# Kernel tuning notes

Hardware: AMD Instinct MI355X
Metric: run time of the kernel (lower is better)

Reference implementation:

```python
import jax, jax.numpy as jnp
import numpy as np

N_IN = 10    # input_dim: x has 2**N_IN features
N_OUT = 10   # output_dim: output has 2**N_OUT features
RANK = 10
BATCH = 512
STD = 0.5


def setup_inputs() -> dict:
    key = jax.random.key(0)
    ks = jax.random.split(key, 5)
    x = jax.random.normal(ks[0], (BATCH, 2 ** N_IN), dtype=jnp.float32)
    # Stacked tensor-train cores; each core is (rank, 2, 2, rank) as in the torch module.
    input_cores = STD * jax.random.normal(ks[1], (N_IN, RANK, 2, 2, RANK), dtype=jnp.float32)
    output_cores = STD * jax.random.normal(ks[2], (N_OUT, RANK, 2, 2, RANK), dtype=jnp.float32)
    # central core is (2,)*(N_IN+N_OUT) in the original; stored here as the
    # equivalent (2**N_IN, 2**N_OUT) matrix (identical math, same memory layout).
    central_core = STD * jax.random.normal(ks[3], (2 ** N_IN, 2 ** N_OUT), dtype=jnp.float32)
    bias = STD * jax.random.normal(ks[4], (1, 2 ** N_OUT), dtype=jnp.float32)
    return {"x": x, "input_cores": input_cores, "output_cores": output_cores,
            "central_core": central_core, "bias": bias}


def reference(x, input_cores, output_cores, central_core, bias):
    # Tensor-wheel contraction with a fixed, precomputed path (replaces the
    # per-call greedy tensornetwork contractor). Exact same sum as the original.
    B = x.shape[0]
    n, r = input_cores.shape[0], input_cores.shape[1]
    m = output_cores.shape[0]

    # --- absorb x into the input-core chain ---
    # State S: (B, l0, C_acc, r_cur, Q_rem) where
    #   l0    = open left bond of input core 0 (closes the ring later)
    #   C_acc = accumulated central-core legs c_1..c_i (dim 2^i, c_1 most significant)
    #   Q_rem = remaining input bits of x (x bit 1 is most significant, matching reshape)
    S = jnp.einsum('bpq,lpcs->blcsq', x.reshape(B, 2, -1), input_cores[0])
    for i in range(1, n):
        _, l, C, rc, Q = S.shape
        S = S.reshape(B, l, C, rc, 2, Q // 2)
        S = jnp.einsum('blcrpq,rpds->blcdsq', S, input_cores[i]).reshape(B, l, 2 * C, r, Q // 2)
    S = S[..., 0]  # (B, l0, 2^n, r_n)

    # --- contract the central core over all input-side legs (dominant GEMM) ---
    U = jnp.einsum('blcr,cd->blrd', S, central_core)  # (B, l0, r_n, 2^m)

    # --- sweep through the output-core chain ---
    # State V: (B, l0, P_acc, r_cur, D_rem); P_acc accumulates free output legs
    # p_1..p_j (p_1 most significant), D_rem holds remaining central output legs.
    V = U.reshape(B, r, 1, r, 2 ** m)
    for j in range(m):
        _, l, P, rc, D = V.shape
        V = V.reshape(B, l, P, rc, 2, D // 2)
        V = jnp.einsum('blxrdq,rpds->blxpsq', V, output_cores[j]).reshape(B, l, 2 * P, r, D // 2)

    # --- close the ring: trace l0 (input core 0 left bond) with rgt_m ---
    out = jnp.einsum('blpl->bp', V[..., 0])  # (B, 2^m)
    return out + bias
```

## Files before the change

kernel.cpp:

```cpp
#include <hip/hip_runtime.h>
#include <cstdint>
#include <cstddef>


typedef __attribute__((ext_vector_type(8))) short short8;
typedef __attribute__((ext_vector_type(4))) float f32x4;

static __device__ __forceinline__ unsigned short f2bf(float f) {
  union { float f; unsigned int u; } v; v.f = f;
  unsigned int r = v.u + 0x7FFFu + ((v.u >> 16) & 1u);
  return (unsigned short)(r >> 16);
}
static __device__ __forceinline__ unsigned int pack2(float a, float b) {
  return (unsigned int)f2bf(a) | ((unsigned int)f2bf(b) << 16);
}

static __device__ __forceinline__ int shuf_in(int stg, int u, int dd) {
  if (stg == 0) return ((u >> 4) << 6) | (dd << 4) | ((u & 3) << 2) | ((u >> 2) & 3);
  if (stg == 1) return ((u >> 2) << 4) | (dd << 2) | (u & 3);
  return (u << 2) | dd;
}
static __device__ __forceinline__ int shuf_out(int stg, int u, int dd) {
  if (stg == 0) return (dd << 6) | ((u & 15) << 2) | (u >> 4);
  if (stg == 1) return ((u >> 4) << 6) | (dd << 4) | ((u & 3) << 2) | ((u >> 2) & 3);
  if (stg == 2) return ((u >> 2) << 4) | (dd << 2) | (u & 3);
  return (u << 2) | dd;
}

static __device__ __forceinline__ void mfma_stage80(
    const unsigned short* stc, const unsigned short* __restrict__ Bf,
    int w, int lane, int c15, int quad, f32x4 acc[4][3]) {
  short8 bfr[3][2];
  #pragma unroll
  for (int nt = 0; nt < 3; ++nt) {
    bfr[nt][0] = *(const short8*)&Bf[(nt * 2 + 0) * 512 + lane * 8];
    bfr[nt][1] = *(const short8*)&Bf[(nt * 2 + 1) * 512 + lane * 8];
  }
  #pragma unroll
  for (int rt = 0; rt < 4; ++rt) {
    const int rowA = w * 64 + rt * 16 + c15;
    const short8 a0 = *(const short8*)((const char*)stc + rowA * 80 + quad * 16);
    const int a1off = (quad == 0) ? rowA * 80 + 64 : 0;
    const short8 a1 = *(const short8*)((const char*)stc + a1off);
    #pragma unroll
    for (int nt = 0; nt < 3; ++nt) {
      f32x4 a = {0.f, 0.f, 0.f, 0.f};
      a = __builtin_amdgcn_mfma_f32_16x16x32_bf16(a0, bfr[nt][0], a, 0, 0, 0);
      a = __builtin_amdgcn_mfma_f32_16x16x32_bf16(a1, bfr[nt][1], a, 0, 0, 0);
      acc[rt][nt] = a;
    }
  }
}

template <int STG, bool INPUT>
static __device__ __forceinline__ void stage_writes80(
    unsigned short* dst, const f32x4 acc[4][3], int w, int quad,
    const int* ddv, const int* sv) {
  #pragma unroll
  for (int rt = 0; rt < 4; ++rt) {
    const int u = w * 16 + rt * 4 + quad;
    #pragma unroll
    for (int nt = 0; nt < 3; ++nt) {
      if (sv[nt] < 10) {
        const int dd = ddv[nt];
        const int row = INPUT ? shuf_in(STG, u, dd) : shuf_out(STG, u, dd);
        uint2 v;
        v.x = pack2(acc[rt][nt][0], acc[rt][nt][1]);
        v.y = pack2(acc[rt][nt][2], acc[rt][nt][3]);
        *(uint2*)((char*)dst + row * 80 + sv[nt] * 8) = v;
      }
    }
  }
}

__global__ __launch_bounds__(256) void k0_prep(
    const float* __restrict__ ic, const float* __restrict__ oc,
    const float* __restrict__ cc, unsigned short* __restrict__ Bt,
    float* __restrict__ c2x, unsigned short* __restrict__ bf1,
    unsigned short* __restrict__ bf3, unsigned short* __restrict__ bf3l) {
  const int t = threadIdx.x;
  const int bx = blockIdx.x;
  if (bx < 1024) {
    const int dly = bx;
    const int D = (dly & 3) * 256 + ((dly >> 2) & 3) * 64 + (dly >> 4);
    const int uC = (t >> 2) * 16 + (t & 3);
    ushort4 pk;
    pk.x = f2bf(cc[(size_t)(uC + 0) * 1024 + D]);
    pk.y = f2bf(cc[(size_t)(uC + 4) * 1024 + D]);
    pk.z = f2bf(cc[(size_t)(uC + 8) * 1024 + D]);
    pk.w = f2bf(cc[(size_t)(uC + 12) * 1024 + D]);
    *(ushort4*)&Bt[(size_t)dly * 1024 + 4 * t] = pk;
  } else if (bx == 1024) {
    for (int idx = t; idx < 1600; idx += 256) {
      int L = idx / 160, rem = idx - L * 160;
      int w = rem / 40, r2 = rem - w * 40;
      int pi = r2 / 10, s = r2 - pi * 10;
      int p1 = pi >> 1, p2 = pi & 1, c1 = w >> 1, c2v = w & 1;
      float a = 0.f;
      for (int r1 = 0; r1 < 10; ++r1)
        a += ic[L * 40 + p1 * 20 + c1 * 10 + r1] *
             ic[400 + r1 * 40 + p2 * 20 + c2v * 10 + s];
      c2x[idx] = a;
    }
  } else if (bx == 1025) {
    for (int idx = t; idx < 12288; idx += 256) {
      int j = idx & 7, lane = (idx >> 3) & 63, kc = (idx >> 9) & 1;
      int g2 = idx >> 10, stg = g2 / 3, nt = g2 - stg * 3;
      int c15 = lane & 15, quad = lane >> 4;
      int n = nt * 16 + c15, dd = n / 12, s = n - dd * 12;
      int k = kc * 32 + quad * 8 + j, c = k >> 2, pi = k & 3;
      float v = 0.f;
      if (k < 40 && s < 10) {
        int p1 = pi >> 1, p2 = pi & 1, d1 = dd >> 1, d2 = dd & 1;
        const float* A = ic + (2 * stg + 2) * 400;
        const float* B = ic + (2 * stg + 3) * 400;
        for (int tt = 0; tt < 10; ++tt)
          v += A[c * 40 + p1 * 20 + d1 * 10 + tt] *
               B[tt * 40 + p2 * 20 + d2 * 10 + s];
      }
      bf1[idx] = f2bf(v);
    }
  } else if (bx == 1026) {
    for (int idx = t; idx < 12288; idx += 256) {
      int j = idx & 7, lane = (idx >> 3) & 63, kc = (idx >> 9) & 1;
      int g2 = idx >> 10, stg = g2 / 3, nt = g2 - stg * 3;
      int c15 = lane & 15, quad = lane >> 4;
      int n = nt * 16 + c15, dd = n / 12, s = n - dd * 12;
      int k = kc * 32 + quad * 8 + j, c = k >> 2, pi = k & 3;
      float v = 0.f;
      if (k < 40 && s < 10) {
        int d1 = pi >> 1, d2 = pi & 1, p1 = dd >> 1, p2 = dd & 1;
        const float* A = oc + (2 * stg) * 400;
        const float* B = oc + (2 * stg + 1) * 400;
        for (int tt = 0; tt < 10; ++tt)
          v += A[c * 40 + p1 * 20 + d1 * 10 + tt] *
               B[tt * 40 + p2 * 20 + d2 * 10 + s];
      }
      bf3[idx] = f2bf(v);
    }
  } else {
    for (int idx = t; idx < 10240; idx += 256) {
      int j = idx & 7, lane = (idx >> 3) & 63, kc = (idx >> 9) & 1, L = idx >> 10;
      int c15 = lane & 15, quad = lane >> 4;
      int k = kc * 32 + quad * 8 + j, c = k >> 2, pi = k & 3;
      float v = 0.f;
      if (k < 40 && c15 < 4) {
        int dd = c15, d1 = pi >> 1, d2 = pi & 1, p1 = dd >> 1, p2 = dd & 1;
        for (int tt = 0; tt < 10; ++tt)
          v += oc[8 * 400 + c * 40 + p1 * 20 + d1 * 10 + tt] *
               oc[9 * 400 + tt * 40 + p2 * 20 + d2 * 10 + L];
      }
      bf3l[idx] = f2bf(v);
    }
  }
}

__global__ __launch_bounds__(256, 4) void k1_insweep(
    const float* __restrict__ x, const float* __restrict__ c2x,
    const unsigned short* __restrict__ bf1, unsigned short* __restrict__ S) {
  __shared__ __align__(16) unsigned short st[20480];
  const int t = threadIdx.x, bx = blockIdx.x;
  const int b = bx / 10, L = bx - b * 10;
  const int lane = t & 63, w = t >> 6;
  const int c15 = lane & 15, quad = lane >> 4;
  int ddv[3], sv[3];
  #pragma unroll
  for (int nt = 0; nt < 3; ++nt) {
    int n = nt * 16 + c15; ddv[nt] = n / 12; sv[nt] = n - ddv[nt] * 12;
  }
  unsigned short* bufA = st;
  unsigned short* bufB = st + 10240;
  {
    const float* xb = x + (size_t)b * 1024;
    const float* C2 = c2x + L * 160 + w * 40;
    float accx[4][10];
    #pragma unroll
    for (int g = 0; g < 4; ++g)
      #pragma unroll
      for (int s = 0; s < 10; ++s) accx[g][s] = 0.f;
    #pragma unroll
    for (int pi = 0; pi < 4; ++pi) {
      float xv[4];
      #pragma unroll
      for (int g = 0; g < 4; ++g) xv[g] = xb[pi * 256 + g * 64 + lane];
      #pragma unroll
      for (int s = 0; s < 10; ++s) {
        const float bv = C2[pi * 10 + s];
        #pragma unroll
        for (int g = 0; g < 4; ++g) accx[g][s] = fmaf(xv[g], bv, accx[g][s]);
      }
    }
    const int row = w * 64 + c15 * 4 + quad;
    #pragma unroll
    for (int s = 0; s < 10; ++s) {
      uint2 v;
      v.x = pack2(accx[0][s], accx[1][s]);
      v.y = pack2(accx[2][s], accx[3][s]);
      *(uint2*)((char*)bufA + row * 80 + s * 8) = v;
    }
  }
  __syncthreads();
  f32x4 acc[4][3];
  mfma_stage80(bufA, bf1 + 0 * 3072, w, lane, c15, quad, acc);
  stage_writes80<0, true>(bufB, acc, w, quad, ddv, sv);
  __syncthreads();
  mfma_stage80(bufB, bf1 + 1 * 3072, w, lane, c15, quad, acc);
  stage_writes80<1, true>(bufA, acc, w, quad, ddv, sv);
  __syncthreads();
  mfma_stage80(bufA, bf1 + 2 * 3072, w, lane, c15, quad, acc);
  stage_writes80<2, true>(bufB, acc, w, quad, ddv, sv);
  __syncthreads();
  mfma_stage80(bufB, bf1 + 3 * 3072, w, lane, c15, quad, acc);
  #pragma unroll
  for (int rt = 0; rt < 4; ++rt) {
    const int u = w * 16 + rt * 4 + quad;
    #pragma unroll
    for (int nt = 0; nt < 3; ++nt) {
      if (sv[nt] < 10) {
        uint2 v;
        v.x = pack2(acc[rt][nt][0], acc[rt][nt][1]);
        v.y = pack2(acc[rt][nt][2], acc[rt][nt][3]);
        *(uint2*)&S[((size_t)(bx * 10 + sv[nt])) * 1024 + u * 16 + ddv[nt] * 4] = v;
      }
    }
  }
}


#define K2_STAGE(T, KS)                                                        \
  {                                                                            \
    const unsigned short* gs = gptr + (T) * 64 + (KS) * 32;                    \
    char* lb = lds_stage + (((T) & 1) << 16) + ((KS) << 15);                   \
    _Pragma("unroll")                                                          \
    for (int i = 0; i < 4; ++i)                                                \
      __builtin_amdgcn_global_load_lds(                                        \
          (const __attribute__((address_space(1))) void*)(gs + (i << 14)),     \
          (__attribute__((address_space(3))) void*)(lb + (i << 10)), 16, 0, 0);\
  }

#define K2_PHASE(T, KS, DO_STAGE, VMCNT_ASM, DO_SYNC)                          \
  {                                                                            \
    const char* rb = ldsb + (((T) & 1) << 16) + ((KS) << 15);                  \
    short8 afr[8], bfr[4];                                                     \
    _Pragma("unroll")                                                          \
    for (int mt = 0; mt < 8; ++mt)                                             \
      afr[mt] = *(const short8*)(rb + ((arow0 + (mt << 4)) << 6) + aswz);      \
    _Pragma("unroll")                                                          \
    for (int nt = 0; nt < 4; ++nt)                                             \
      bfr[nt] = *(const short8*)(rb + 16384 + ((brow0 + (nt << 4)) << 6) + aswz);\
    __builtin_amdgcn_s_setprio(1);                                             \
    _Pragma("unroll")                                                          \
    for (int mt = 0; mt < 8; ++mt)                                             \
      _Pragma("unroll")                                                        \
      for (int nt = 0; nt < 4; ++nt)                                           \
        acc[mt][nt] = __builtin_amdgcn_mfma_f32_16x16x32_bf16(                 \
            afr[mt], bfr[nt], acc[mt][nt], 0, 0, 0);                           \
    __builtin_amdgcn_s_setprio(0);                                             \
    if (DO_SYNC) {                                                             \
      asm volatile("s_waitcnt lgkmcnt(0)" ::: "memory");                       \
      __builtin_amdgcn_sched_barrier(0);                                       \
      __builtin_amdgcn_s_barrier();         \
      __builtin_amdgcn_sched_barrier(0);                                       \
      if (DO_STAGE) K2_STAGE((T) + 2, (KS))                                    \
      __builtin_amdgcn_sched_barrier(0);                                       \
      VMCNT_ASM;                             \
      __builtin_amdgcn_s_barrier();              \
      __builtin_amdgcn_sched_barrier(0);                                       \
    }                                                                          \
  }

__global__ __launch_bounds__(512, 2) void k2_gemm(
    const unsigned short* __restrict__ A,
    const unsigned short* __restrict__ B,
    unsigned short* __restrict__ U2a,
    unsigned short* __restrict__ U2b) {
  __shared__ __align__(16) char ldsb[131072];
  const int tid = threadIdx.x, bx = blockIdx.x;
  const int bid = (bx & 7) * 100 + (bx >> 3);
  const int bm = bid & 3, bn = bid >> 2;
  const int Mtile0 = bm << 8, Ntile0 = bn << 8;
  const int w = tid >> 6, lane = tid & 63;
  const int c15 = lane & 15, quad = lane >> 4;
  const int wm = w >> 2, wn = w & 3;

  const int arow0 = (wm << 7) + c15;
  const int brow0 = (wn << 6) + c15;
  const int aswz = ((quad ^ ((c15 >> 1) & 3)) << 4);

  const int sec = w >> 2;
  const int rsub = ((w & 3) << 6) + (lane >> 2);
  const unsigned short* gbase =
      (sec == 0) ? (A + ((size_t)(Mtile0 + rsub) << 10))
                 : (B + ((size_t)(Ntile0 + rsub) << 10));
  const unsigned short* gptr = gbase + (((lane & 3) ^ ((lane >> 3) & 3)) << 3);
  char* lds_stage = ldsb + (sec << 14) + ((w & 3) << 12);

  f32x4 acc[8][4];
  #pragma unroll
  for (int i = 0; i < 8; ++i)
    #pragma unroll
    for (int j = 0; j < 4; ++j) acc[i][j] = (f32x4){0.f, 0.f, 0.f, 0.f};

  K2_STAGE(0, 0)
  K2_STAGE(0, 1)
  K2_STAGE(1, 0)
  K2_STAGE(1, 1)
  asm volatile("s_waitcnt vmcnt(12)" ::: "memory");
  __builtin_amdgcn_s_barrier();
  __builtin_amdgcn_sched_barrier(0);

  #define K2_VM12 asm volatile("s_waitcnt vmcnt(12)" ::: "memory")
  #pragma unroll 2
  for (int kt = 0; kt < 14; ++kt) {
    K2_PHASE(kt, 0, true, K2_VM12, true)
    K2_PHASE(kt, 1, true, K2_VM12, true)
  }
  K2_PHASE(14, 0, false, asm volatile("s_waitcnt vmcnt(8)" ::: "memory"), true)
  K2_PHASE(14, 1, false, asm volatile("s_waitcnt vmcnt(4)" ::: "memory"), true)
  K2_PHASE(15, 0, false, asm volatile("s_waitcnt vmcnt(0)" ::: "memory"), true)
  K2_PHASE(15, 1, false, (void)0, false)

  const int col0 = Ntile0 + (wn << 6) + c15;
  const int rowb = Mtile0 + (wm << 7);
  #pragma unroll
  for (int nt = 0; nt < 4; ++nt) {
    const int n = col0 + (nt << 4);
    const int bl = n / 10;
    const int r = n - bl * 10;
    char* dst = (r < 8)
        ? (char*)U2a + (size_t)bl * 16384 + (size_t)r * 8
        : (char*)U2b + (size_t)bl * 4096 + (size_t)(r - 8) * 8;
    const int rbs = (r < 8) ? 64 : 16;
    #pragma unroll
    for (int mt = 0; mt < 8; ++mt) {
      const int mp = (rowb + (mt << 4) + (quad << 2)) >> 2;
      uint2 v;
      v.x = pack2(acc[mt][nt][0], acc[mt][nt][1]);
      v.y = pack2(acc[mt][nt][2], acc[mt][nt][3]);
      *(uint2*)(dst + (size_t)mp * rbs) = v;
    }
  }
}

__global__ __launch_bounds__(256, 4) void k3_outsweep(
    const unsigned short* __restrict__ U2a, const unsigned short* __restrict__ U2b,
    const unsigned short* __restrict__ bf3, const unsigned short* __restrict__ bf3l,
    const float* __restrict__ bias, float* __restrict__ out) {
  __shared__ __align__(16) unsigned short st[20480];
  const int t = threadIdx.x, bx = blockIdx.x;
  const int b = bx / 10, L = bx - b * 10;
  const int lane = t & 63, w = t >> 6;
  const int c15 = lane & 15, quad = lane >> 4;
  int ddv[3], sv[3];
  #pragma unroll
  for (int nt = 0; nt < 3; ++nt) {
    int n = nt * 16 + c15; ddv[nt] = n / 12; sv[nt] = n - ddv[nt] * 12;
  }
  unsigned short* bufA = st;
  unsigned short* bufB = st + 10240;
  f32x4 acc[4][3];
  {
    short8 bfr[3][2];
    #pragma unroll
    for (int nt = 0; nt < 3; ++nt) {
      bfr[nt][0] = *(const short8*)&bf3[(nt * 2 + 0) * 512 + lane * 8];
      bfr[nt][1] = *(const short8*)&bf3[(nt * 2 + 1) * 512 + lane * 8];
    }
    const char* Ua = (const char*)U2a + (size_t)bx * 16384;
    const char* Ub = (const char*)U2b + (size_t)bx * 4096;
    #pragma unroll
    for (int rt = 0; rt < 4; ++rt) {
      const int m = w * 64 + rt * 16 + c15;
      const short8 a0 = *(const short8*)(Ua + m * 64 + quad * 16);
      const short8 a1 = *(const short8*)(Ub + m * 16);
      #pragma unroll
      for (int nt = 0; nt < 3; ++nt) {
        f32x4 a = {0.f, 0.f, 0.f, 0.f};
        a = __builtin_amdgcn_mfma_f32_16x16x32_bf16(a0, bfr[nt][0], a, 0, 0, 0);
        a = __builtin_amdgcn_mfma_f32_16x16x32_bf16(a1, bfr[nt][1], a, 0, 0, 0);
        acc[rt][nt] = a;
      }
    }
    stage_writes80<0, false>(bufA, acc, w, quad, ddv, sv);
  }
  __syncthreads();
  mfma_stage80(bufA, bf3 + 1 * 3072, w, lane, c15, quad, acc);
  stage_writes80<1, false>(bufB, acc, w, quad, ddv, sv);
  __syncthreads();
  mfma_stage80(bufB, bf3 + 2 * 3072, w, lane, c15, quad, acc);
  stage_writes80<2, false>(bufA, acc, w, quad, ddv, sv);
  __syncthreads();
  mfma_stage80(bufA, bf3 + 3 * 3072, w, lane, c15, quad, acc);
  stage_writes80<3, false>(bufB, acc, w, quad, ddv, sv);
  __syncthreads();
  {
    const unsigned short* Bf = bf3l + L * 1024;
    const short8 b0 = *(const short8*)&Bf[lane * 8];
    const short8 b1 = *(const short8*)&Bf[512 + lane * 8];
    #pragma unroll
    for (int rt = 0; rt < 4; ++rt) {
      const int rowA = w * 64 + rt * 16 + c15;
      const short8 a0 = *(const short8*)((const char*)bufB + rowA * 80 + quad * 16);
      const int a1off = (quad == 0) ? rowA * 80 + 64 : 0;
      const short8 a1 = *(const short8*)((const char*)bufB + a1off);
      f32x4 a = {0.f, 0.f, 0.f, 0.f};
      a = __builtin_amdgcn_mfma_f32_16x16x32_bf16(a0, b0, a, 0, 0, 0);
      a = __builtin_amdgcn_mfma_f32_16x16x32_bf16(a1, b1, a, 0, 0, 0);
      if (c15 < 4) {
        const int u = w * 16 + rt * 4 + quad;
        #pragma unroll
        for (int i = 0; i < 4; ++i) {
          const int oidx = u * 16 + i * 4 + c15;
          float v = a[i];
          if (L == 0) v += bias[oidx];
          atomicAdd(&out[(size_t)b * 1024 + oidx], v);
        }
      }
    }
  }
}

extern "C" void kernel_launch(void* const* d_in, const int* in_sizes, int n_in,
                              void* d_out, int out_size, void* d_ws, size_t ws_size,
                              hipStream_t stream) {
  (void)in_sizes; (void)n_in; (void)ws_size;
  const float* x    = (const float*)d_in[0];
  const float* ic   = (const float*)d_in[1];
  const float* oc   = (const float*)d_in[2];
  const float* cc   = (const float*)d_in[3];
  const float* bias = (const float*)d_in[4];
  float* out = (float*)d_out;

  char* ws = (char*)d_ws;
  unsigned short* S    = (unsigned short*)(ws);
  unsigned short* U2a  = (unsigned short*)(ws + 104857600);
  unsigned short* U2b  = (unsigned short*)(ws + 188743680);
  unsigned short* Bt   = (unsigned short*)(ws + 209715200);
  float*          c2x  = (float*)(ws + 211812352);
  unsigned short* bf1  = (unsigned short*)(ws + 211818752);
  unsigned short* bf3  = (unsigned short*)(ws + 211843328);
  unsigned short* bf3l = (unsigned short*)(ws + 211867904);

  hipMemsetAsync(d_out, 0, (size_t)out_size * sizeof(float), stream);
  k0_prep<<<1028, 256, 0, stream>>>(ic, oc, cc, Bt, c2x, bf1, bf3, bf3l);
  k1_insweep<<<5120, 256, 0, stream>>>(x, c2x, bf1, S);
  k2_gemm<<<800, 512, 0, stream>>>(Bt, S, U2a, U2b);
  k3_outsweep<<<5120, 256, 0, stream>>>(U2a, U2b, bf3, bf3l, bias, out);
}
```

Baseline: 362.3 us.

## Restructure GEMM into 256x128 tiles with triple-buffered LDS ring pipeline

Measured after the change: 339.3 us (median of 2 runs). 1.07x faster.

```diff
diff --git a/kernel.cpp b/kernel.cpp
--- a/kernel.cpp
+++ b/kernel.cpp
@@ -227,20 +227,21 @@
 }
 
 
-#define K2_STAGE(T, KS)                                                        \
+#define K2_STAGE6(SLOT)                                                        \
   {                                                                            \
-    const unsigned short* gs = gptr + (T) * 64 + (KS) * 32;                    \
-    char* lb = lds_stage + (((T) & 1) << 16) + ((KS) << 15);                   \
+    char* lb = ldsb + (SLOT) * 24576 + w * 6144;                               \
     _Pragma("unroll")                                                          \
-    for (int i = 0; i < 4; ++i)                                                \
+    for (int i = 0; i < 6; ++i) {                                              \
       __builtin_amdgcn_global_load_lds(                                        \
-          (const __attribute__((address_space(1))) void*)(gs + (i << 14)),     \
+          (const __attribute__((address_space(1))) void*)(gsrc[i]),            \
           (__attribute__((address_space(3))) void*)(lb + (i << 10)), 16, 0, 0);\
-  }
-
-#define K2_PHASE(T, KS, DO_STAGE, VMCNT_ASM, DO_SYNC)                          \
+      gsrc[i] += 32;                            \
+    }                                                                          \
+  }
+
+#define K2_PHASE(RSLOT, SSLOT, DO_STAGE, VMCNT_ASM, DO_SYNC)                   \
   {                                                                            \
-    const char* rb = ldsb + (((T) & 1) << 16) + ((KS) << 15);                  \
+    const char* rb = ldsb + (RSLOT) * 24576;                                   \
     short8 afr[8], bfr[4];                                                     \
     _Pragma("unroll")                                                          \
     for (int mt = 0; mt < 8; ++mt)                                             \
@@ -248,6 +249,7 @@
     _Pragma("unroll")                                                          \
     for (int nt = 0; nt < 4; ++nt)                                             \
       bfr[nt] = *(const short8*)(rb + 16384 + ((brow0 + (nt << 4)) << 6) + aswz);\
+    if (DO_STAGE) K2_STAGE6(SSLOT)                                             \
     __builtin_amdgcn_s_setprio(1);                                             \
     _Pragma("unroll")                                                          \
     for (int mt = 0; mt < 8; ++mt)                                             \
@@ -257,43 +259,43 @@
             afr[mt], bfr[nt], acc[mt][nt], 0, 0, 0);                           \
     __builtin_amdgcn_s_setprio(0);                                             \
     if (DO_SYNC) {                                                             \
-      asm volatile("s_waitcnt lgkmcnt(0)" ::: "memory");                       \
-      __builtin_amdgcn_sched_barrier(0);                                       \
-      __builtin_amdgcn_s_barrier();         \
-      __builtin_amdgcn_sched_barrier(0);                                       \
-      if (DO_STAGE) K2_STAGE((T) + 2, (KS))                                    \
-      __builtin_amdgcn_sched_barrier(0);                                       \
-      VMCNT_ASM;                             \
-      __builtin_amdgcn_s_barrier();              \
+      VMCNT_ASM;                                \
+      __builtin_amdgcn_s_barrier();             \
       __builtin_amdgcn_sched_barrier(0);                                       \
     }                                                                          \
   }
 
-__global__ __launch_bounds__(512, 2) void k2_gemm(
+#define K2_VM6 asm volatile("s_waitcnt vmcnt(6)" ::: "memory")
+#define K2_VM0 asm volatile("s_waitcnt vmcnt(0)" ::: "memory")
+
+__global__ __launch_bounds__(256, 2) void k2_gemm(
     const unsigned short* __restrict__ A,
     const unsigned short* __restrict__ B,
     unsigned short* __restrict__ U2a,
     unsigned short* __restrict__ U2b) {
-  __shared__ __align__(16) char ldsb[131072];
+  __shared__ __align__(16) char ldsb[73728];
   const int tid = threadIdx.x, bx = blockIdx.x;
-  const int bid = (bx & 7) * 100 + (bx >> 3);
+  const int bid = (bx & 7) * 200 + (bx >> 3);
   const int bm = bid & 3, bn = bid >> 2;
-  const int Mtile0 = bm << 8, Ntile0 = bn << 8;
+  const int Mtile0 = bm << 8, Ntile0 = bn << 7;
   const int w = tid >> 6, lane = tid & 63;
   const int c15 = lane & 15, quad = lane >> 4;
-  const int wm = w >> 2, wn = w & 3;
+  const int wm = w >> 1, wn = w & 1;
 
   const int arow0 = (wm << 7) + c15;
   const int brow0 = (wn << 6) + c15;
   const int aswz = ((quad ^ ((c15 >> 1) & 3)) << 4);
 
-  const int sec = w >> 2;
-  const int rsub = ((w & 3) << 6) + (lane >> 2);
-  const unsigned short* gbase =
-      (sec == 0) ? (A + ((size_t)(Mtile0 + rsub) << 10))
-                 : (B + ((size_t)(Ntile0 + rsub) << 10));
-  const unsigned short* gptr = gbase + (((lane & 3) ^ ((lane >> 3) & 3)) << 3);
-  char* lds_stage = ldsb + (sec << 14) + ((w & 3) << 12);
+  const unsigned short* gsrc[6];
+  #pragma unroll
+  for (int i = 0; i < 6; ++i) {
+    const int rowc = w * 96 + i * 16;
+    const int row = rowc + (lane >> 2);
+    const unsigned short* g = (rowc < 256)
+        ? (A + ((size_t)(Mtile0 + row) << 10))
+        : (B + ((size_t)(Ntile0 + row - 256) << 10));
+    gsrc[i] = g + (((lane & 3) ^ ((lane >> 3) & 3)) << 3);
+  }
 
   f32x4 acc[8][4];
   #pragma unroll
@@ -301,24 +303,20 @@
     #pragma unroll
     for (int j = 0; j < 4; ++j) acc[i][j] = (f32x4){0.f, 0.f, 0.f, 0.f};
 
-  K2_STAGE(0, 0)
-  K2_STAGE(0, 1)
-  K2_STAGE(1, 0)
-  K2_STAGE(1, 1)
-  asm volatile("s_waitcnt vmcnt(12)" ::: "memory");
+  K2_STAGE6(0)
+  K2_STAGE6(1)
+  K2_VM6;
   __builtin_amdgcn_s_barrier();
   __builtin_amdgcn_sched_barrier(0);
 
-  #define K2_VM12 asm volatile("s_waitcnt vmcnt(12)" ::: "memory")
-  #pragma unroll 2
-  for (int kt = 0; kt < 14; ++kt) {
-    K2_PHASE(kt, 0, true, K2_VM12, true)
-    K2_PHASE(kt, 1, true, K2_VM12, true)
-  }
-  K2_PHASE(14, 0, false, asm volatile("s_waitcnt vmcnt(8)" ::: "memory"), true)
-  K2_PHASE(14, 1, false, asm volatile("s_waitcnt vmcnt(4)" ::: "memory"), true)
-  K2_PHASE(15, 0, false, asm volatile("s_waitcnt vmcnt(0)" ::: "memory"), true)
-  K2_PHASE(15, 1, false, (void)0, false)
+  #pragma unroll 1
+  for (int it = 0; it < 10; ++it) {
+    K2_PHASE(0, 2, true, K2_VM6, true)
+    K2_PHASE(1, 0, true, K2_VM6, true)
+    K2_PHASE(2, 1, true, K2_VM6, true)
+  }
+  K2_PHASE(0, 2, false, K2_VM0, true)
+  K2_PHASE(1, 2, false, (void)0, false)
 
   const int col0 = Ntile0 + (wn << 6) + c15;
   const int rowb = Mtile0 + (wm << 7);
@@ -444,6 +442,6 @@
   hipMemsetAsync(d_out, 0, (size_t)out_size * sizeof(float), stream);
   k0_prep<<<1028, 256, 0, stream>>>(ic, oc, cc, Bt, c2x, bf1, bf3, bf3l);
   k1_insweep<<<5120, 256, 0, stream>>>(x, c2x, bf1, S);
-  k2_gemm<<<800, 512, 0, stream>>>(Bt, S, U2a, U2b);
+  k2_gemm<<<1600, 256, 0, stream>>>(Bt, S, U2a, U2b);
   k3_outsweep<<<5120, 256, 0, stream>>>(U2a, U2b, bf3, bf3l, bias, out);
 }
```
